# Performance work log

Hardware: AMD Instinct MI355X
Metric: run time of the kernel (lower is better)

The kernel has to match this reference:

```python
import jax, jax.numpy as jnp
import numpy as np

D_IN = 1024
D_OUT = 1024

def setup_inputs() -> dict:
    key = jax.random.key(0)
    k1, k2, k3, k4 = jax.random.split(key, 4)
    x = jax.random.normal(k1, (4, 2048, D_IN), dtype=jnp.float32)
    s = 1.0 / np.sqrt(D_IN)
    Wk = jax.random.normal(k2, (D_OUT, D_IN), dtype=jnp.float32) * s
    Wq = jax.random.normal(k3, (D_OUT, D_IN), dtype=jnp.float32) * s
    Wv = jax.random.normal(k4, (D_OUT, D_IN), dtype=jnp.float32) * s
    return {"x": x, "Wk": Wk, "Wq": Wq, "Wv": Wv}

def reference(x, Wk, Wq, Wv):
    # Note: original code applies k_w to produce 'weighted_q' and q_w for
    # 'weighted_k' (swapped names); we reproduce the exact math.
    b, s, _ = x.shape
    q = jnp.einsum('bsd,ed->bse', x, Wk)  # [B,S,d_out]
    k = jnp.einsum('bsd,ed->bse', x, Wq)  # [B,S,d_out]
    v = jnp.einsum('bsd,ed->bse', x, Wv)  # [B,S,d_out]
    scores = jnp.einsum('bqe,bke->bqk', q, k)  # [B,S,S]
    causal = jnp.triu(jnp.ones((s, s), dtype=bool), k=1)  # True = masked (future)
    scores = jnp.where(causal[None], -jnp.inf, scores)
    inv_sqrt_d = jnp.float32(1.0 / np.sqrt(Wk.shape[0]))
    attn = jax.nn.softmax(scores * inv_sqrt_d, axis=-1)
    return jnp.einsum('bqk,bke->bqe', attn, v)
```

## Files before the change

### kernel.cpp

```cpp
#include <hip/hip_runtime.h>
#include <hip/hip_bf16.h>
#include <stdint.h>

#define BATCH 4
#define SEQ   2048
#define DIN   1024
#define DOUT  1024
#define MTOT  (BATCH*SEQ)

typedef __attribute__((ext_vector_type(8))) short bf16x8;
typedef __attribute__((ext_vector_type(4))) float f32x4;
typedef unsigned short ushort_t;

__device__ inline unsigned short f2bf(float f) {
  union { float f; unsigned u; } a; a.f = f;
  unsigned r = a.u + 0x7fffu + ((a.u >> 16) & 1u);
  return (unsigned short)(r >> 16);
}
__device__ inline float bf2f(unsigned short b) {
  union { unsigned u; float f; } a; a.u = ((unsigned)b) << 16; return a.f;
}

__device__ inline void gload_lds16(const void* g, void* l) {
  __builtin_amdgcn_global_load_lds(
      (__attribute__((address_space(1))) void*)(uintptr_t)(g),
      (__attribute__((address_space(3))) void*)(uintptr_t)(l),
      16, 0, 0);
}

__global__ __launch_bounds__(256)
void convert_kernel(const float* __restrict__ x, const float* __restrict__ wk,
                    const float* __restrict__ wq, const float* __restrict__ wv,
                    unsigned short* __restrict__ xb, unsigned short* __restrict__ wkqb,
                    unsigned short* __restrict__ wvb) {
  const long NX = (long)MTOT * DIN;
  const long NW = (long)DOUT * DIN;
  long t = (long)blockIdx.x * blockDim.x + threadIdx.x;
  long off = t * 4;
  if (off >= NX + 3 * NW) return;
  const float* src; unsigned short* dst; long o;
  if (off < NX)            { src = x;  dst = xb;        o = off; }
  else if (off < NX + NW)  { src = wk; dst = wkqb;      o = off - NX; }
  else if (off < NX + 2*NW){ src = wq; dst = wkqb + NW; o = off - NX - NW; }
  else                     { src = wv; dst = wvb;       o = off - NX - 2*NW; }
  f32x4 v = *(const f32x4*)(src + o);
  unsigned p0 = (unsigned)f2bf(v[0]) | ((unsigned)f2bf(v[1]) << 16);
  unsigned p1 = (unsigned)f2bf(v[2]) | ((unsigned)f2bf(v[3]) << 16);
  uint2* d = (uint2*)(dst + o);
  *d = make_uint2(p0, p1);
}

#define GBM 256
#define GBN 128
#define GBK 64

__device__ inline void stage3(const unsigned short* __restrict__ Ab,
                              const unsigned short* __restrict__ Bb,
                              int lda, int ldb, int k0,
                              unsigned short* at, unsigned short* bt, int tid) {
#pragma unroll
  for (int i = 0; i < 4; i++) {
    int idx = i * 512 + tid;
    int row = idx >> 3;
    int cb  = (idx & 7) << 4;
    int cbs = cb ^ ((row & 7) << 4);
    gload_lds16((const char*)Ab + (long)row * (lda * 2) + k0 * 2 + cbs,
                (char*)at + idx * 16);
  }
#pragma unroll
  for (int i = 0; i < 2; i++) {
    int idx = i * 512 + tid;
    int row = idx >> 3;
    int cb  = (idx & 7) << 4;
    int cbs = cb ^ ((row & 7) << 4);
    gload_lds16((const char*)Bb + (long)row * (ldb * 2) + k0 * 2 + cbs,
                (char*)bt + idx * 16);
  }
}

__device__ inline void compute3(const unsigned short* at, const unsigned short* bt,
                                int lane, int wm, int wn, f32x4 acc[4][4]) {
#pragma unroll
  for (int kk = 0; kk < 2; kk++) {
    bf16x8 af[4], bfr[4];
#pragma unroll
    for (int ii = 0; ii < 4; ii++) {
      int row = wm * 64 + ii * 16 + (lane & 15);
      int cb  = (kk * 64 + ((lane >> 4) << 4)) ^ ((row & 7) << 4);
      af[ii] = *(const bf16x8*)((const char*)at + row * 128 + cb);
    }
#pragma unroll
    for (int j = 0; j < 4; j++) {
      int row = wn * 64 + j * 16 + (lane & 15);
      int cb  = (kk * 64 + ((lane >> 4) << 4)) ^ ((row & 7) << 4);
      bfr[j] = *(const bf16x8*)((const char*)bt + row * 128 + cb);
    }
    __builtin_amdgcn_s_setprio(1);
#pragma unroll
    for (int ii = 0; ii < 4; ii++)
#pragma unroll
      for (int j = 0; j < 4; j++)
        acc[ii][j] = __builtin_amdgcn_mfma_f32_16x16x32_bf16(af[ii], bfr[j], acc[ii][j], 0, 0, 0);
    __builtin_amdgcn_s_setprio(0);
  }
}

__global__ __launch_bounds__(512, 2)
void gemm3_kernel(const unsigned short* __restrict__ A,
                  const unsigned short* __restrict__ Bw,
                  unsigned short* __restrict__ C,
                  int lda, int ldb, int ldc, int K) {
  __shared__ unsigned short at[3][GBM * GBK];
  __shared__ unsigned short bt[3][GBN * GBK];
  const int bj = blockIdx.x, bi = blockIdx.y;
  const unsigned short* Ab = A + (long)bi * GBM * lda;
  const unsigned short* Bb = Bw + (long)bj * GBN * ldb;
  const int tid = threadIdx.x, lane = tid & 63, w = tid >> 6;
  const int wm = w >> 1, wn = w & 1;

  f32x4 acc[4][4];
#pragma unroll
  for (int i = 0; i < 4; i++)
#pragma unroll
    for (int j = 0; j < 4; j++) acc[i][j] = (f32x4){0.f, 0.f, 0.f, 0.f};

  const int nt = K / GBK;
  unsigned short *a0 = at[0], *a1 = at[1], *a2 = at[2];
  unsigned short *b0 = bt[0], *b1 = bt[1], *b2 = bt[2];

  stage3(Ab, Bb, lda, ldb, 0,      a0, b0, tid);
  stage3(Ab, Bb, lda, ldb, GBK,    a1, b1, tid);

  for (int t = 0; t < nt; t++) {
    if (t + 2 < nt) stage3(Ab, Bb, lda, ldb, (t + 2) * GBK, a2, b2, tid);
    asm volatile("s_waitcnt vmcnt(12)" ::: "memory");
    __builtin_amdgcn_s_barrier();
    asm volatile("" ::: "memory");
    compute3(a0, b0, lane, wm, wn, acc);
    asm volatile("" ::: "memory");
    __builtin_amdgcn_s_barrier();
    unsigned short* ta = a0; a0 = a1; a1 = a2; a2 = ta;
    unsigned short* tb = b0; b0 = b1; b1 = b2; b2 = tb;
  }

  const long crow0 = (long)bi * GBM + wm * 64;
  const long ccol0 = (long)bj * GBN + wn * 64;
#pragma unroll
  for (int i = 0; i < 4; i++) {
    const long row0 = crow0 + i * 16 + ((lane >> 4) << 2);
#pragma unroll
    for (int j = 0; j < 4; j++) {
      const long col = ccol0 + j * 16 + (lane & 15);
#pragma unroll
      for (int r2 = 0; r2 < 4; r2++)
        C[(row0 + r2) * ldc + col] = f2bf(acc[i][j][r2]);
    }
  }
}

#define BM 128
#define BN 128
#define BK 64

__global__ __launch_bounds__(256, 2)
void gemm_kernel(const unsigned short* __restrict__ A,
                 const unsigned short* __restrict__ Bw,
                 void* __restrict__ Cout,
                 int lda, int ldb, int ldc, int K,
                 long aBatch, long bBatch, long cBatch,
                 float scale, int outBf16, int triPack, int klimit, int balance) {
  int bj = blockIdx.x, bi = blockIdx.y, b = blockIdx.z;
  if (triPack) {
    int idx = blockIdx.x;
    int t = (int)((sqrtf(8.f * idx + 1.f) - 1.f) * 0.5f);
    while ((t + 1) * (t + 2) / 2 <= idx) t++;
    while (t * (t + 1) / 2 > idx) t--;
    bi = t; bj = idx - t * (t + 1) / 2;
  }
  if (balance) {
    int y = bi, h = y >> 1;
    y = (y & 1) ? 15 - h : h;
    if (b >= 2) y = 15 - y;
    bi = y;
  }
  int Keff = K;
  if (klimit) { int km = (bi + 1) * BM; Keff = km < K ? km : K; }

  const unsigned short* Ab = A  + (long)b * aBatch + (long)bi * BM * lda;
  const unsigned short* Bb = Bw + (long)b * bBatch + (long)bj * BN * ldb;

  __shared__ unsigned short at[BM * BK];
  __shared__ unsigned short bt[BN * BK];

  const int tid  = threadIdx.x;
  const int lane = tid & 63;
  const int w    = tid >> 6;
  const int wm   = w >> 1;
  const int wn   = w & 1;

  f32x4 acc[4][4];
#pragma unroll
  for (int i = 0; i < 4; i++)
#pragma unroll
    for (int j = 0; j < 4; j++) acc[i][j] = (f32x4){0.f, 0.f, 0.f, 0.f};

  const int srow = lane >> 3;
  const int scol = (lane & 7) * 8;

  const int ntiles = Keff / BK;
  for (int kt = 0; kt < ntiles; ++kt) {
    const int k0 = kt * BK;
    if (kt) __syncthreads();
#pragma unroll
    for (int t = 0; t < 4; t++) {
      const int r = w * 32 + t * 8 + srow;
      gload_lds16(Ab + (long)r * lda + k0 + scol, &at[(w * 32 + t * 8) * BK + lane * 8]);
      gload_lds16(Bb + (long)r * ldb + k0 + scol, &bt[(w * 32 + t * 8) * BK + lane * 8]);
    }
    asm volatile("s_waitcnt vmcnt(0)" ::: "memory");
    __syncthreads();
#pragma unroll
    for (int kk = 0; kk < 2; ++kk) {
      bf16x8 af[4], bfr[4];
#pragma unroll
      for (int i = 0; i < 4; i++)
        af[i] = *(const bf16x8*)&at[(wm * 64 + i * 16 + (lane & 15)) * BK + kk * 32 + (lane >> 4) * 8];
#pragma unroll
      for (int j = 0; j < 4; j++)
        bfr[j] = *(const bf16x8*)&bt[(wn * 64 + j * 16 + (lane & 15)) * BK + kk * 32 + (lane >> 4) * 8];
#pragma unroll
      for (int i = 0; i < 4; i++)
#pragma unroll
        for (int j = 0; j < 4; j++)
          acc[i][j] = __builtin_amdgcn_mfma_f32_16x16x32_bf16(af[i], bfr[j], acc[i][j], 0, 0, 0);
    }
  }

  const long crow0 = (long)bi * BM + wm * 64;
  const long ccol0 = (long)bj * BN + wn * 64;
  if (outBf16) {
    unsigned short* C = (unsigned short*)Cout + (long)b * cBatch;
#pragma unroll
    for (int i = 0; i < 4; i++) {
      const long row0 = crow0 + i * 16 + ((lane >> 4) << 2);
#pragma unroll
      for (int j = 0; j < 4; j++) {
        const long col = ccol0 + j * 16 + (lane & 15);
#pragma unroll
        for (int r2 = 0; r2 < 4; r2++)
          C[(row0 + r2) * ldc + col] = f2bf(acc[i][j][r2] * scale);
      }
    }
  } else {
    float* C = (float*)Cout + (long)b * cBatch;
#pragma unroll
    for (int i = 0; i < 4; i++) {
      const long row0 = crow0 + i * 16 + ((lane >> 4) << 2);
#pragma unroll
      for (int j = 0; j < 4; j++) {
        const long col = ccol0 + j * 16 + (lane & 15);
#pragma unroll
        for (int r2 = 0; r2 < 4; r2++)
          C[(row0 + r2) * ldc + col] = acc[i][j][r2] * scale;
      }
    }
  }
}

__global__ __launch_bounds__(256)
void transpose_kernel(const unsigned short* __restrict__ qkv, unsigned short* __restrict__ vtb) {
  __shared__ unsigned short lds[64][65];
  const int m0 = blockIdx.x * 64, e0 = blockIdx.y * 64;
  const int t = threadIdx.x;
  const int r = t >> 3, c = (t & 7) * 8;
#pragma unroll
  for (int h = 0; h < 2; h++) {
    const int rr = r + h * 32;
    uint4 raw = *(const uint4*)(qkv + (long)(m0 + rr) * 3072 + 2048 + e0 + c);
    const unsigned short* u = (const unsigned short*)&raw;
#pragma unroll
    for (int k = 0; k < 8; k++) lds[rr][c + k] = u[k];
  }
  __syncthreads();
#pragma unroll
  for (int h = 0; h < 2; h++) {
    const int er = r + h * 32;
    unsigned short v[8];
#pragma unroll
    for (int k = 0; k < 8; k++) v[k] = lds[c + k][er];
    *(uint4*)(vtb + (long)(e0 + er) * 8192 + m0 + c) = *(const uint4*)v;
  }
}

__global__ __launch_bounds__(256)
void softmax_kernel(const unsigned short* __restrict__ scores, unsigned short* __restrict__ P) {
  const int w = threadIdx.x >> 6, lane = threadIdx.x & 63;
  const int r = blockIdx.x * 4 + w;
  const int i = r & (SEQ - 1);
  const int kend = ((i >> 7) + 1) << 7;
  const unsigned short* src = scores + (long)r * SEQ;
  unsigned short* dst = P + (long)r * SEQ;

  float e[4][8];
  float m = -1e30f;
#pragma unroll
  for (int c = 0; c < 4; c++) {
    const int j0 = c * 512 + lane * 8;
    if (j0 < kend) {
      uint4 raw = *(const uint4*)(src + j0);
      const unsigned short* u = (const unsigned short*)&raw;
#pragma unroll
      for (int k = 0; k < 8; k++) {
        float v = bf2f(u[k]);
        e[c][k] = (j0 + k <= i) ? v : -1e30f;
        m = fmaxf(m, e[c][k]);
      }
    } else {
#pragma unroll
      for (int k = 0; k < 8; k++) e[c][k] = -1e30f;
    }
  }
#pragma unroll
  for (int o = 32; o; o >>= 1) m = fmaxf(m, __shfl_xor(m, o, 64));

  float s = 0.f;
#pragma unroll
  for (int c = 0; c < 4; c++)
#pragma unroll
    for (int k = 0; k < 8; k++) {
      float x = (e[c][k] > -1e29f) ? __expf(e[c][k] - m) : 0.f;
      e[c][k] = x; s += x;
    }
#pragma unroll
  for (int o = 32; o; o >>= 1) s += __shfl_xor(s, o, 64);
  const float inv = 1.0f / s;

#pragma unroll
  for (int c = 0; c < 4; c++) {
    const int j0 = c * 512 + lane * 8;
    if (j0 < kend) {
      unsigned short v[8];
#pragma unroll
      for (int k = 0; k < 8; k++) v[k] = f2bf(e[c][k] * inv);
      *(uint4*)(dst + j0) = *(const uint4*)v;
    }
  }
}

extern "C" void kernel_launch(void* const* d_in, const int* in_sizes, int n_in,
                              void* d_out, int out_size, void* d_ws, size_t ws_size,
                              hipStream_t stream) {
  const float* x  = (const float*)d_in[0];
  const float* Wk = (const float*)d_in[1];
  const float* Wq = (const float*)d_in[2];
  const float* Wv = (const float*)d_in[3];

  char* ws = (char*)d_ws;
  unsigned short* xb      = (unsigned short*)(ws);
  unsigned short* qkv     = (unsigned short*)(ws + 16777216);
  unsigned short* vtb     = (unsigned short*)(ws + 67108864);
  unsigned short* wb      = (unsigned short*)(ws + 83886080);
  unsigned short* scoresb = (unsigned short*)(ws + 90177536);
  unsigned short* P       = (unsigned short*)(ws + 123731968);
  float* out = (float*)d_out;

  {
    long total4 = ((long)MTOT * DIN + 3L * DOUT * DIN) / 4;
    int blocks = (int)((total4 + 255) / 256);
    convert_kernel<<<dim3(blocks), dim3(256), 0, stream>>>(x, Wk, Wq, Wv, xb, wb, wb + 2 * 1048576);
  }
  gemm3_kernel<<<dim3(3072 / GBN, 8192 / GBM), dim3(512), 0, stream>>>(
      xb, wb, qkv, 1024, 1024, 3072, 1024);
  transpose_kernel<<<dim3(8192 / 64, 1024 / 64), dim3(256), 0, stream>>>(qkv, vtb);
  gemm_kernel<<<dim3(136, 1, BATCH), dim3(256), 0, stream>>>(
      qkv, qkv + 1024, scoresb, 3072, 3072, 2048, 1024,
      (long)SEQ * 3072, (long)SEQ * 3072, (long)SEQ * SEQ, 0.03125f, 1, 1, 0, 0);
  softmax_kernel<<<dim3(BATCH * SEQ / 4), dim3(256), 0, stream>>>(scoresb, P);
  gemm_kernel<<<dim3(1024 / BN, 2048 / BM, BATCH), dim3(256), 0, stream>>>(
      P, vtb, out, 2048, 8192, 1024, 2048,
      (long)SEQ * SEQ, 2048L, (long)SEQ * DOUT, 1.0f, 0, 0, 1, 1);
}
```

Measured before the change: 255.9 us.

## Unify GEMMs into one 256x128 ping-pong kernel with interleaved prefetch

Replaces the triple-buffered QKV GEMM and the 128x128 batched GEMM with a single 256x128-tile, 512-thread kernel. It double-buffers LDS and issues the next tile's A and B loads between MFMA phases, with barriers separating the row groups. It also adds an XCD-style block swizzle for the QKV GEMM and a 256x128 triangular packing for the scores GEMM, which now uses 72 instead of 136 blocks per batch. The PV GEMM no longer limits K to the causal extent, and softmax now writes zeros past kend so P is fully defined. That trades skipped work and the deeper prefetch for bigger tiles and better overlap.

```diff
diff --git a/kernel.cpp b/kernel.cpp
--- a/kernel.cpp
+++ b/kernel.cpp
@@ -10,7 +10,6 @@
 
 typedef __attribute__((ext_vector_type(8))) short bf16x8;
 typedef __attribute__((ext_vector_type(4))) float f32x4;
-typedef unsigned short ushort_t;
 
 __device__ inline unsigned short f2bf(float f) {
   union { float f; unsigned u; } a; a.f = f;
@@ -50,194 +49,139 @@
   *d = make_uint2(p0, p1);
 }
 
-#define GBM 256
-#define GBN 128
-#define GBK 64
-
-__device__ inline void stage3(const unsigned short* __restrict__ Ab,
-                              const unsigned short* __restrict__ Bb,
-                              int lda, int ldb, int k0,
-                              unsigned short* at, unsigned short* bt, int tid) {
-#pragma unroll
-  for (int i = 0; i < 4; i++) {
-    int idx = i * 512 + tid;
+__device__ inline void stage8A(const unsigned short* __restrict__ Ab, int ldab,
+                               int k0b, unsigned short* at, int tid) {
+#pragma unroll
+  for (int u = 0; u < 4; u++) {
+    int idx = u * 512 + tid;
     int row = idx >> 3;
     int cb  = (idx & 7) << 4;
     int cbs = cb ^ ((row & 7) << 4);
-    gload_lds16((const char*)Ab + (long)row * (lda * 2) + k0 * 2 + cbs,
+    gload_lds16((const char*)Ab + (long)row * ldab + k0b + cbs,
                 (char*)at + idx * 16);
   }
-#pragma unroll
-  for (int i = 0; i < 2; i++) {
-    int idx = i * 512 + tid;
+}
+__device__ inline void stage8B(const unsigned short* __restrict__ Bb, int ldbb,
+                               int k0b, unsigned short* bt, int tid) {
+#pragma unroll
+  for (int u = 0; u < 2; u++) {
+    int idx = u * 512 + tid;
     int row = idx >> 3;
     int cb  = (idx & 7) << 4;
     int cbs = cb ^ ((row & 7) << 4);
-    gload_lds16((const char*)Bb + (long)row * (ldb * 2) + k0 * 2 + cbs,
+    gload_lds16((const char*)Bb + (long)row * ldbb + k0b + cbs,
                 (char*)bt + idx * 16);
   }
 }
 
-__device__ inline void compute3(const unsigned short* at, const unsigned short* bt,
-                                int lane, int wm, int wn, f32x4 acc[4][4]) {
-#pragma unroll
-  for (int kk = 0; kk < 2; kk++) {
-    bf16x8 af[4], bfr[4];
-#pragma unroll
-    for (int ii = 0; ii < 4; ii++) {
-      int row = wm * 64 + ii * 16 + (lane & 15);
-      int cb  = (kk * 64 + ((lane >> 4) << 4)) ^ ((row & 7) << 4);
-      af[ii] = *(const bf16x8*)((const char*)at + row * 128 + cb);
-    }
+__global__ __launch_bounds__(512, 2)
+void gemm8_kernel(const unsigned short* __restrict__ A,
+                  const unsigned short* __restrict__ Bw,
+                  void* __restrict__ Cout,
+                  int lda, int ldb, int ldc, int K,
+                  long aBatch, long bBatch, long cBatch,
+                  float scale, int outBf16, int tri, int swiz) {
+  __shared__ unsigned short at[2][256 * 64];
+  __shared__ unsigned short bt[2][128 * 64];
+  int bi, bj;
+  const int b = blockIdx.z;
+  if (tri) {
+    int idx = blockIdx.x;
+    int R = (int)((sqrtf(4.f * idx + 1.f) - 1.f) * 0.5f);
+    while ((R + 1) * (R + 2) <= idx) R++;
+    while (R * (R + 1) > idx) R--;
+    bi = R; bj = idx - R * (R + 1);
+  } else if (swiz) {
+    int nx = gridDim.x;
+    int wg = blockIdx.y * nx + blockIdx.x;
+    int nwg = nx * gridDim.y;
+    int q = nwg >> 3;
+    int s = (wg & 7) * q + (wg >> 3);
+    bi = s / nx; bj = s % nx;
+  } else { bi = blockIdx.y; bj = blockIdx.x; }
+
+  const unsigned short* Ab = A  + (long)b * aBatch + (long)bi * 256 * lda;
+  const unsigned short* Bb = Bw + (long)b * bBatch + (long)bj * 128 * ldb;
+  const int ldab = lda * 2, ldbb = ldb * 2;
+  const int tid = threadIdx.x, lane = tid & 63, w = tid >> 6;
+  const int wm = w >> 1, wn = w & 1;
+
+  f32x4 acc[4][4];
+#pragma unroll
+  for (int i = 0; i < 4; i++)
+#pragma unroll
+    for (int j = 0; j < 4; j++) acc[i][j] = (f32x4){0.f, 0.f, 0.f, 0.f};
+
+  stage8A(Ab, ldab, 0, at[0], tid);
+  stage8B(Bb, ldbb, 0, bt[0], tid);
+
+  const int nt = K / 64;
+  for (int t = 0; t < nt; ++t) {
+    const unsigned short* a  = at[t & 1];
+    const unsigned short* bb = bt[t & 1];
+    unsigned short* an = at[(t & 1) ^ 1];
+    unsigned short* bn = bt[(t & 1) ^ 1];
+    const int last = (t + 1 >= nt);
+    const int k0b = (t + 1) * 128;
+
+    asm volatile("s_waitcnt vmcnt(0)" ::: "memory");
+    __builtin_amdgcn_s_barrier();
+    asm volatile("" ::: "memory");
+
+    bf16x8 bf[4][2];
 #pragma unroll
     for (int j = 0; j < 4; j++) {
       int row = wn * 64 + j * 16 + (lane & 15);
-      int cb  = (kk * 64 + ((lane >> 4) << 4)) ^ ((row & 7) << 4);
-      bfr[j] = *(const bf16x8*)((const char*)bt + row * 128 + cb);
-    }
+#pragma unroll
+      for (int kk = 0; kk < 2; kk++) {
+        int cb = (kk * 64 + ((lane >> 4) << 4)) ^ ((row & 7) << 4);
+        bf[j][kk] = *(const bf16x8*)((const char*)bb + row * 128 + cb);
+      }
+    }
+    bf16x8 af0[2];
+    {
+      int row = wm * 64 + (lane & 15);
+#pragma unroll
+      for (int kk = 0; kk < 2; kk++) {
+        int cb = (kk * 64 + ((lane >> 4) << 4)) ^ ((row & 7) << 4);
+        af0[kk] = *(const bf16x8*)((const char*)a + row * 128 + cb);
+      }
+    }
+    if (!last) stage8A(Ab, ldab, k0b, an, tid);
+    __builtin_amdgcn_s_barrier();
     __builtin_amdgcn_s_setprio(1);
 #pragma unroll
-    for (int ii = 0; ii < 4; ii++)
+    for (int kk = 0; kk < 2; kk++)
 #pragma unroll
       for (int j = 0; j < 4; j++)
-        acc[ii][j] = __builtin_amdgcn_mfma_f32_16x16x32_bf16(af[ii], bfr[j], acc[ii][j], 0, 0, 0);
+        acc[0][j] = __builtin_amdgcn_mfma_f32_16x16x32_bf16(af0[kk], bf[j][kk], acc[0][j], 0, 0, 0);
     __builtin_amdgcn_s_setprio(0);
-  }
-}
-
-__global__ __launch_bounds__(512, 2)
-void gemm3_kernel(const unsigned short* __restrict__ A,
-                  const unsigned short* __restrict__ Bw,
-                  unsigned short* __restrict__ C,
-                  int lda, int ldb, int ldc, int K) {
-  __shared__ unsigned short at[3][GBM * GBK];
-  __shared__ unsigned short bt[3][GBN * GBK];
-  const int bj = blockIdx.x, bi = blockIdx.y;
-  const unsigned short* Ab = A + (long)bi * GBM * lda;
-  const unsigned short* Bb = Bw + (long)bj * GBN * ldb;
-  const int tid = threadIdx.x, lane = tid & 63, w = tid >> 6;
-  const int wm = w >> 1, wn = w & 1;
-
-  f32x4 acc[4][4];
-#pragma unroll
-  for (int i = 0; i < 4; i++)
-#pragma unroll
-    for (int j = 0; j < 4; j++) acc[i][j] = (f32x4){0.f, 0.f, 0.f, 0.f};
-
-  const int nt = K / GBK;
-  unsigned short *a0 = at[0], *a1 = at[1], *a2 = at[2];
-  unsigned short *b0 = bt[0], *b1 = bt[1], *b2 = bt[2];
-
-  stage3(Ab, Bb, lda, ldb, 0,      a0, b0, tid);
-  stage3(Ab, Bb, lda, ldb, GBK,    a1, b1, tid);
-
-  for (int t = 0; t < nt; t++) {
-    if (t + 2 < nt) stage3(Ab, Bb, lda, ldb, (t + 2) * GBK, a2, b2, tid);
-    asm volatile("s_waitcnt vmcnt(12)" ::: "memory");
     __builtin_amdgcn_s_barrier();
-    asm volatile("" ::: "memory");
-    compute3(a0, b0, lane, wm, wn, acc);
-    asm volatile("" ::: "memory");
-    __builtin_amdgcn_s_barrier();
-    unsigned short* ta = a0; a0 = a1; a1 = a2; a2 = ta;
-    unsigned short* tb = b0; b0 = b1; b1 = b2; b2 = tb;
-  }
-
-  const long crow0 = (long)bi * GBM + wm * 64;
-  const long ccol0 = (long)bj * GBN + wn * 64;
-#pragma unroll
-  for (int i = 0; i < 4; i++) {
-    const long row0 = crow0 + i * 16 + ((lane >> 4) << 2);
-#pragma unroll
-    for (int j = 0; j < 4; j++) {
-      const long col = ccol0 + j * 16 + (lane & 15);
-#pragma unroll
-      for (int r2 = 0; r2 < 4; r2++)
-        C[(row0 + r2) * ldc + col] = f2bf(acc[i][j][r2]);
-    }
-  }
-}
-
-#define BM 128
-#define BN 128
-#define BK 64
-
-__global__ __launch_bounds__(256, 2)
-void gemm_kernel(const unsigned short* __restrict__ A,
-                 const unsigned short* __restrict__ Bw,
-                 void* __restrict__ Cout,
-                 int lda, int ldb, int ldc, int K,
-                 long aBatch, long bBatch, long cBatch,
-                 float scale, int outBf16, int triPack, int klimit, int balance) {
-  int bj = blockIdx.x, bi = blockIdx.y, b = blockIdx.z;
-  if (triPack) {
-    int idx = blockIdx.x;
-    int t = (int)((sqrtf(8.f * idx + 1.f) - 1.f) * 0.5f);
-    while ((t + 1) * (t + 2) / 2 <= idx) t++;
-    while (t * (t + 1) / 2 > idx) t--;
-    bi = t; bj = idx - t * (t + 1) / 2;
-  }
-  if (balance) {
-    int y = bi, h = y >> 1;
-    y = (y & 1) ? 15 - h : h;
-    if (b >= 2) y = 15 - y;
-    bi = y;
-  }
-  int Keff = K;
-  if (klimit) { int km = (bi + 1) * BM; Keff = km < K ? km : K; }
-
-  const unsigned short* Ab = A  + (long)b * aBatch + (long)bi * BM * lda;
-  const unsigned short* Bb = Bw + (long)b * bBatch + (long)bj * BN * ldb;
-
-  __shared__ unsigned short at[BM * BK];
-  __shared__ unsigned short bt[BN * BK];
-
-  const int tid  = threadIdx.x;
-  const int lane = tid & 63;
-  const int w    = tid >> 6;
-  const int wm   = w >> 1;
-  const int wn   = w & 1;
-
-  f32x4 acc[4][4];
-#pragma unroll
-  for (int i = 0; i < 4; i++)
-#pragma unroll
-    for (int j = 0; j < 4; j++) acc[i][j] = (f32x4){0.f, 0.f, 0.f, 0.f};
-
-  const int srow = lane >> 3;
-  const int scol = (lane & 7) * 8;
-
-  const int ntiles = Keff / BK;
-  for (int kt = 0; kt < ntiles; ++kt) {
-    const int k0 = kt * BK;
-    if (kt) __syncthreads();
-#pragma unroll
-    for (int t = 0; t < 4; t++) {
-      const int r = w * 32 + t * 8 + srow;
-      gload_lds16(Ab + (long)r * lda + k0 + scol, &at[(w * 32 + t * 8) * BK + lane * 8]);
-      gload_lds16(Bb + (long)r * ldb + k0 + scol, &bt[(w * 32 + t * 8) * BK + lane * 8]);
-    }
-    asm volatile("s_waitcnt vmcnt(0)" ::: "memory");
-    __syncthreads();
-#pragma unroll
-    for (int kk = 0; kk < 2; ++kk) {
-      bf16x8 af[4], bfr[4];
-#pragma unroll
-      for (int i = 0; i < 4; i++)
-        af[i] = *(const bf16x8*)&at[(wm * 64 + i * 16 + (lane & 15)) * BK + kk * 32 + (lane >> 4) * 8];
-#pragma unroll
-      for (int j = 0; j < 4; j++)
-        bfr[j] = *(const bf16x8*)&bt[(wn * 64 + j * 16 + (lane & 15)) * BK + kk * 32 + (lane >> 4) * 8];
-#pragma unroll
-      for (int i = 0; i < 4; i++)
+
+#pragma unroll
+    for (int q = 1; q < 4; q++) {
+      bf16x8 afq[2];
+      int row = wm * 64 + q * 16 + (lane & 15);
+#pragma unroll
+      for (int kk = 0; kk < 2; kk++) {
+        int cb = (kk * 64 + ((lane >> 4) << 4)) ^ ((row & 7) << 4);
+        afq[kk] = *(const bf16x8*)((const char*)a + row * 128 + cb);
+      }
+      if (q == 1 && !last) stage8B(Bb, ldbb, k0b, bn, tid);
+      __builtin_amdgcn_s_barrier();
+      __builtin_amdgcn_s_setprio(1);
+#pragma unroll
+      for (int kk = 0; kk < 2; kk++)
 #pragma unroll
         for (int j = 0; j < 4; j++)
-          acc[i][j] = __builtin_amdgcn_mfma_f32_16x16x32_bf16(af[i], bfr[j], acc[i][j], 0, 0, 0);
-    }
-  }
-
-  const long crow0 = (long)bi * BM + wm * 64;
-  const long ccol0 = (long)bj * BN + wn * 64;
+          acc[q][j] = __builtin_amdgcn_mfma_f32_16x16x32_bf16(afq[kk], bf[j][kk], acc[q][j], 0, 0, 0);
+      __builtin_amdgcn_s_setprio(0);
+      __builtin_amdgcn_s_barrier();
+    }
+  }
+
+  const long crow0 = (long)bi * 256 + wm * 64;
+  const long ccol0 = (long)bj * 128 + wn * 64;
   if (outBf16) {
     unsigned short* C = (unsigned short*)Cout + (long)b * cBatch;
 #pragma unroll
@@ -338,12 +282,10 @@
 #pragma unroll
   for (int c = 0; c < 4; c++) {
     const int j0 = c * 512 + lane * 8;
-    if (j0 < kend) {
-      unsigned short v[8];
-#pragma unroll
-      for (int k = 0; k < 8; k++) v[k] = f2bf(e[c][k] * inv);
-      *(uint4*)(dst + j0) = *(const uint4*)v;
-    }
+    unsigned short v[8];
+#pragma unroll
+    for (int k = 0; k < 8; k++) v[k] = f2bf(e[c][k] * inv);
+    *(uint4*)(dst + j0) = *(const uint4*)v;
   }
 }
 
@@ -369,14 +311,14 @@
     int blocks = (int)((total4 + 255) / 256);
     convert_kernel<<<dim3(blocks), dim3(256), 0, stream>>>(x, Wk, Wq, Wv, xb, wb, wb + 2 * 1048576);
   }
-  gemm3_kernel<<<dim3(3072 / GBN, 8192 / GBM), dim3(512), 0, stream>>>(
-      xb, wb, qkv, 1024, 1024, 3072, 1024);
+  gemm8_kernel<<<dim3(3072 / 128, 8192 / 256, 1), dim3(512), 0, stream>>>(
+      xb, wb, qkv, 1024, 1024, 3072, 1024, 0L, 0L, 0L, 1.0f, 1, 0, 1);
   transpose_kernel<<<dim3(8192 / 64, 1024 / 64), dim3(256), 0, stream>>>(qkv, vtb);
-  gemm_kernel<<<dim3(136, 1, BATCH), dim3(256), 0, stream>>>(
+  gemm8_kernel<<<dim3(72, 1, BATCH), dim3(512), 0, stream>>>(
       qkv, qkv + 1024, scoresb, 3072, 3072, 2048, 1024,
-      (long)SEQ * 3072, (long)SEQ * 3072, (long)SEQ * SEQ, 0.03125f, 1, 1, 0, 0);
+      (long)SEQ * 3072, (long)SEQ * 3072, (long)SEQ * SEQ, 0.03125f, 1, 1, 0);
   softmax_kernel<<<dim3(BATCH * SEQ / 4), dim3(256), 0, stream>>>(scoresb, P);
-  gemm_kernel<<<dim3(1024 / BN, 2048 / BM, BATCH), dim3(256), 0, stream>>>(
+  gemm8_kernel<<<dim3(1024 / 128, 2048 / 256, BATCH), dim3(512), 0, stream>>>(
       P, vtb, out, 2048, 8192, 1024, 2048,
-      (long)SEQ * SEQ, 2048L, (long)SEQ * DOUT, 1.0f, 0, 0, 1, 1);
-}
+      (long)SEQ * SEQ, 2048L, (long)SEQ * DOUT, 1.0f, 0, 0, 1);
+}
```

New measurement: 253.4 us. Within noise of the previous version (-1.0%).
